# Optimization experiments

Hardware: AMD Instinct MI355X
Metric: run time of the kernel (lower is better)

Reference implementation:

```python
import jax, jax.numpy as jnp
import numpy as np

B, L, R, D = 64, 512, 512, 512
F_CONV, H = 100, 60

def setup_inputs() -> dict:
    key = jax.random.key(0)
    ks = jax.random.split(key, 8)
    l_lengths = jax.random.randint(ks[0], (B,), L // 2, L + 1)
    r_lengths = jax.random.randint(ks[1], (B,), R // 2, R + 1)
    l_vectors = jax.random.normal(ks[2], (L, B, D), jnp.float32)
    r_vectors = jax.random.normal(ks[3], (R, B, D), jnp.float32)
    Wconv = jax.random.normal(ks[4], (F_CONV, D), jnp.float32) / np.sqrt(D).astype(np.float32)
    bconv = jnp.zeros((F_CONV,), jnp.float32)
    Wd = jax.random.normal(ks[5], (H, 2 * F_CONV), jnp.float32) / np.sqrt(2 * F_CONV).astype(np.float32)
    bd = jnp.zeros((H,), jnp.float32)
    return {"l_lengths": l_lengths, "l_vectors": l_vectors, "r_lengths": r_lengths,
            "r_vectors": r_vectors, "Wconv": Wconv, "bconv": bconv, "Wd": Wd, "bd": bd}

def reference(l_lengths, l_vectors, r_lengths, r_vectors, Wconv, bconv, Wd, bd):
    Lm, Bm, Dm = l_vectors.shape
    Rm = r_vectors.shape[0]
    # masks, seq-first [L,B] like pad_sequence output
    l_mask = (jnp.arange(Lm)[:, None] < l_lengths[None, :]).astype(l_vectors.dtype)
    r_mask = (jnp.arange(Rm)[:, None] < r_lengths[None, :]).astype(r_vectors.dtype)
    lmT, rmT = l_mask.T, r_mask.T  # [B,L], [B,R]

    # co-attention scores [B,L,R]
    attention = jnp.einsum('lbd,rbd->blr', l_vectors, r_vectors)
    attention = attention * lmT[:, :, None] * rmT[:, None, :]

    att_r = jax.nn.softmax(attention - 10.0 * (1.0 - lmT[:, :, None]), axis=1)
    att_r = att_r * lmT[:, :, None]
    att_r = att_r / (att_r.sum(axis=1, keepdims=True) + 1e-13)

    att_l = jax.nn.softmax(attention - 10.0 * (1.0 - rmT[:, None, :]), axis=2)
    att_l = att_l * rmT[:, None, :]
    att_l = att_l / (att_l.sum(axis=2, keepdims=True) + 1e-13)

    # ---- left side: stats + top-1 hard attention ----
    rl = r_lengths.astype(l_vectors.dtype)[:, None]
    l_mean = att_l.sum(axis=2) / rl                              # [B,L]
    l_w = (att_l * att_l).sum(axis=2) / rl - l_mean * l_mean
    l_w = l_w / jnp.maximum(l_mean, 0.001)
    l_a = att_l.max(axis=2)                                      # top-1 value [B,L]
    l_i = att_l.argmax(axis=2)                                   # top-1 index [B,L]
    l_i = l_i * lmT.astype(l_i.dtype)
    l_a = l_a / jnp.maximum(l_a, 0.001)                          # k=1: sum == value
    gathered = jnp.take_along_axis(r_vectors, l_i.T[:, :, None], axis=0)  # [L,B,D]
    l_counter = l_a.T[:, :, None] * gathered
    l_c = l_w.T[:, :, None] * jnp.abs(l_vectors - l_counter) * l_mask[:, :, None]

    # ---- right side ----
    ll = l_lengths.astype(r_vectors.dtype)[:, None]
    r_mean = att_r.sum(axis=1) / ll                              # [B,R]
    r_w = (att_r * att_r).sum(axis=1) / ll - r_mean * r_mean
    r_w = r_w / jnp.maximum(r_mean, 0.001)
    r_a = att_r.max(axis=1)                                      # [B,R]
    r_i = att_r.argmax(axis=1)
    r_i = r_i * rmT.astype(r_i.dtype)
    r_a = r_a / jnp.maximum(r_a, 0.001)
    gathered_r = jnp.take_along_axis(l_vectors, r_i.T[:, :, None], axis=0)  # [R,B,D]
    r_counter = r_a.T[:, :, None] * gathered_r
    r_c = r_w.T[:, :, None] * jnp.abs(r_vectors - r_counter) * r_mask[:, :, None]

    # SentenceConv(1, 100, dim): kernel (1, dim) conv == per-position linear,
    # ReLU, masked max-pool over the sequence.
    def sconv(x, mask):  # x [S,B,D], mask [S,B]
        h = jax.nn.relu(jnp.einsum('sbd,fd->bsf', x, Wconv) + bconv)  # [B,S,F]
        h = h - (1.0 - mask.T)[:, :, None] * 1e9
        return h.max(axis=1)  # [B,F]

    feats = jnp.concatenate([sconv(l_c, l_mask), sconv(r_c, r_mask)], axis=1)  # [B,200]
    return jax.nn.relu(feats @ Wd.T + bd)  # [B,60]
```

## Files before the change

### kernel.cpp

```cpp
#include <hip/hip_runtime.h>
#include <math.h>

#define BB 64
#define LL 512
#define RR 512
#define DD 512
#define FC 100
#define FP 112
#define HH 60
#define BD (BB*DD)

typedef __attribute__((ext_vector_type(8))) short bf16x8;
typedef __attribute__((ext_vector_type(4))) float f32x4;

__device__ __forceinline__ unsigned short bf16rne(float x) {
  unsigned u = __float_as_uint(x);
  return (unsigned short)((u + 0x7fffu + ((u >> 16) & 1u)) >> 16);
}
__device__ __forceinline__ float bf16tof(unsigned short h) {
  return __uint_as_float((unsigned)h << 16);
}

__device__ __forceinline__ void split2(float x0, float x1, unsigned& h2, unsigned& l2) {
  unsigned u0 = __float_as_uint(x0), u1 = __float_as_uint(x1);
  h2 = __builtin_amdgcn_perm(u1, u0, 0x07060302u);
  float r0 = x0 - __uint_as_float(u0 & 0xffff0000u);
  float r1 = x1 - __uint_as_float(u1 & 0xffff0000u);
  l2 = __builtin_amdgcn_perm(__float_as_uint(r1), __float_as_uint(r0), 0x07060302u);
}

__global__ __launch_bounds__(512, 2) void gemm_att(const float* __restrict__ lv,
                                                   const float* __restrict__ rv,
                                                   const int* __restrict__ llen,
                                                   const int* __restrict__ rlen,
                                                   float* __restrict__ lpart,
                                                   float* __restrict__ rpart) {
  __shared__ unsigned short Ah[256][40];
  __shared__ unsigned short Al[256][40];
  __shared__ unsigned short Bh[256][40];
  __shared__ unsigned short Bl[256][40];

  const int bid = blockIdx.x;
  const int wid = (bid & 7) * 32 + (bid >> 3);
  const int b  = wid >> 2;
  const int l0 = ((wid >> 1) & 1) * 256;
  const int r0 = (wid & 1) * 256;

  const int t = threadIdx.x;
  const int srow = t >> 1;
  const int half = t & 1;
  const int kq = half * 16;

  const float* Abase = lv + (size_t)(l0 + srow) * BD + b * DD + kq;
  const float* Bbase = rv + (size_t)(r0 + srow) * BD + b * DD + kq;

  float4 pa[4], pb[4];
#pragma unroll
  for (int q = 0; q < 4; ++q) {
    pa[q] = *(const float4*)(Abase + q * 4);
    pb[q] = *(const float4*)(Bbase + q * 4);
  }

  const int lane = t & 63;
  const int wv = t >> 6;
  const int wrow = wv >> 2;
  const int wcol = wv & 3;
  const int fr = lane & 15;
  const int kh = lane >> 4;

  f32x4 acc[8][4];
#pragma unroll
  for (int i = 0; i < 8; ++i)
#pragma unroll
    for (int j = 0; j < 4; ++j) acc[i][j] = (f32x4){0.f, 0.f, 0.f, 0.f};

  for (int it = 0; it < 16; ++it) {
    __syncthreads();
#pragma unroll
    for (int q = 0; q < 4; ++q) {
      unsigned h01, l01, h23, l23;
      split2(pa[q].x, pa[q].y, h01, l01);
      split2(pa[q].z, pa[q].w, h23, l23);
      *(uint2*)&Ah[srow][kq + q * 4] = make_uint2(h01, h23);
      *(uint2*)&Al[srow][kq + q * 4] = make_uint2(l01, l23);
      split2(pb[q].x, pb[q].y, h01, l01);
      split2(pb[q].z, pb[q].w, h23, l23);
      *(uint2*)&Bh[srow][kq + q * 4] = make_uint2(h01, h23);
      *(uint2*)&Bl[srow][kq + q * 4] = make_uint2(l01, l23);
    }
    if (it < 15) {
      const float* An = Abase + (it + 1) * 32;
      const float* Bn = Bbase + (it + 1) * 32;
#pragma unroll
      for (int q = 0; q < 4; ++q) {
        pa[q] = *(const float4*)(An + q * 4);
        pb[q] = *(const float4*)(Bn + q * 4);
      }
    }
    __syncthreads();

    bf16x8 bh[4], bl[4];
#pragma unroll
    for (int j = 0; j < 4; ++j) {
      bh[j] = *(const bf16x8*)&Bh[wcol * 64 + j * 16 + fr][kh * 8];
      bl[j] = *(const bf16x8*)&Bl[wcol * 64 + j * 16 + fr][kh * 8];
    }
#pragma unroll
    for (int i = 0; i < 8; ++i) {
      bf16x8 ah = *(const bf16x8*)&Ah[wrow * 128 + i * 16 + fr][kh * 8];
      bf16x8 al = *(const bf16x8*)&Al[wrow * 128 + i * 16 + fr][kh * 8];
#pragma unroll
      for (int j = 0; j < 4; ++j) {
        acc[i][j] = __builtin_amdgcn_mfma_f32_16x16x32_bf16(ah, bh[j], acc[i][j], 0, 0, 0);
        acc[i][j] = __builtin_amdgcn_mfma_f32_16x16x32_bf16(ah, bl[j], acc[i][j], 0, 0, 0);
        acc[i][j] = __builtin_amdgcn_mfma_f32_16x16x32_bf16(al, bh[j], acc[i][j], 0, 0, 0);
      }
    }
  }

  const int ll_ = llen[b], rl_ = rlen[b];
  __syncthreads();
  float* rowsc = (float*)&Ah[0][0];
  float* colsc = (float*)&Bh[0][0];

#pragma unroll
  for (int i = 0; i < 8; ++i) {
#pragma unroll
    for (int q = 0; q < 4; ++q) {
      const int lrow = wrow * 128 + i * 16 + kh * 4 + q;
      const bool vl = (l0 + lrow) < ll_;
      float s[4];
      float M = -1e30f, bS = -1e30f; int bI = 0;
#pragma unroll
      for (int j = 0; j < 4; ++j) {
        int r = r0 + wcol * 64 + j * 16 + fr;
        bool vr = r < rl_;
        float raw = acc[i][j][q];
        s[j] = !vr ? -10.f : (vl ? raw : 0.f);
        M = fmaxf(M, s[j]);
        if (vr && s[j] > bS) { bS = s[j]; bI = r; }
      }
#pragma unroll
      for (int m = 1; m < 16; m <<= 1) M = fmaxf(M, __shfl_xor(M, m, 64));
      float z0 = 0.f, zv = 0.f, q2 = 0.f;
#pragma unroll
      for (int j = 0; j < 4; ++j) {
        float e = __expf(s[j] - M);
        z0 += e;
        int r = r0 + wcol * 64 + j * 16 + fr;
        if (r < rl_) { zv += e; q2 += e * e; }
      }
#pragma unroll
      for (int m = 1; m < 16; m <<= 1) {
        z0 += __shfl_xor(z0, m, 64);
        zv += __shfl_xor(zv, m, 64);
        q2 += __shfl_xor(q2, m, 64);
        float oS = __shfl_xor(bS, m, 64);
        int   oI = __shfl_xor(bI, m, 64);
        if (oS > bS || (oS == bS && oI < bI)) { bS = oS; bI = oI; }
      }
      if (fr == 0) {
        float* p = rowsc + (wcol * 256 + lrow) * 6;
        p[0] = M; p[1] = z0; p[2] = zv; p[3] = q2; p[4] = bS; p[5] = __int_as_float(bI);
      }
    }
  }

#pragma unroll
  for (int j = 0; j < 4; ++j) {
    const int ccol = wcol * 64 + j * 16 + fr;
    const bool vr = (r0 + ccol) < rl_;
    float M = -1e30f, bS = -1e30f; int bI = 0;
#pragma unroll
    for (int i = 0; i < 8; ++i)
#pragma unroll
      for (int q = 0; q < 4; ++q) {
        int lg = l0 + wrow * 128 + i * 16 + kh * 4 + q;
        bool vl = lg < ll_;
        float raw = acc[i][j][q];
        float sv = !vl ? -10.f : (vr ? raw : 0.f);
        M = fmaxf(M, sv);
        if (vl && sv > bS) { bS = sv; bI = lg; }
      }
    float z0 = 0.f, zv = 0.f, q2 = 0.f;
#pragma unroll
    for (int i = 0; i < 8; ++i)
#pragma unroll
      for (int q = 0; q < 4; ++q) {
        int lg = l0 + wrow * 128 + i * 16 + kh * 4 + q;
        bool vl = lg < ll_;
        float raw = acc[i][j][q];
        float sv = !vl ? -10.f : (vr ? raw : 0.f);
        float e = __expf(sv - M);
        z0 += e;
        if (vl) { zv += e; q2 += e * e; }
      }
#pragma unroll
    for (int m = 16; m < 64; m <<= 1) {
      float oM = __shfl_xor(M, m, 64);
      float oz0 = __shfl_xor(z0, m, 64);
      float ozv = __shfl_xor(zv, m, 64);
      float oq2 = __shfl_xor(q2, m, 64);
      float oS = __shfl_xor(bS, m, 64);
      int   oI = __shfl_xor(bI, m, 64);
      float Mn = fmaxf(M, oM);
      float c0 = __expf(M - Mn), c1 = __expf(oM - Mn);
      z0 = z0 * c0 + oz0 * c1;
      zv = zv * c0 + ozv * c1;
      q2 = q2 * c0 * c0 + oq2 * c1 * c1;
      M = Mn;
      if (oS > bS || (oS == bS && oI < bI)) { bS = oS; bI = oI; }
    }
    if (kh == 0) {
      float* p = colsc + (wrow * 256 + ccol) * 6;
      p[0] = M; p[1] = z0; p[2] = zv; p[3] = q2; p[4] = bS; p[5] = __int_as_float(bI);
    }
  }

  __syncthreads();

  if (t < 256) {
    const float* p = rowsc + t * 6;
    float M = p[0], z0 = p[1], zv = p[2], q2 = p[3], bS = p[4];
    int bI = __float_as_int(p[5]);
#pragma unroll
    for (int w2 = 1; w2 < 4; ++w2) {
      const float* pp = rowsc + (w2 * 256 + t) * 6;
      float M1 = pp[0], z01 = pp[1], zv1 = pp[2], q21 = pp[3], bS1 = pp[4];
      int bI1 = __float_as_int(pp[5]);
      float Mn = fmaxf(M, M1);
      float c0 = __expf(M - Mn), c1 = __expf(M1 - Mn);
      z0 = z0 * c0 + z01 * c1;
      zv = zv * c0 + zv1 * c1;
      q2 = q2 * c0 * c0 + q21 * c1 * c1;
      M = Mn;
      if (bS1 > bS || (bS1 == bS && bI1 < bI)) { bS = bS1; bI = bI1; }
    }
    const int l = l0 + t;
    float* dst = lpart + (((size_t)(b * 512 + l)) * 2 + (r0 >> 8)) * 6;
    *(float2*)(dst + 0) = make_float2(M, z0);
    *(float2*)(dst + 2) = make_float2(zv, q2);
    *(float2*)(dst + 4) = make_float2(bS, __int_as_float(bI));
  } else {
    const int c = t - 256;
    const float* p = colsc + c * 6;
    float M = p[0], z0 = p[1], zv = p[2], q2 = p[3], bS = p[4];
    int bI = __float_as_int(p[5]);
    {
      const float* pp = colsc + (256 + c) * 6;
      float M1 = pp[0], z01 = pp[1], zv1 = pp[2], q21 = pp[3], bS1 = pp[4];
      int bI1 = __float_as_int(pp[5]);
      float Mn = fmaxf(M, M1);
      float c0 = __expf(M - Mn), c1 = __expf(M1 - Mn);
      z0 = z0 * c0 + z01 * c1;
      zv = zv * c0 + zv1 * c1;
      q2 = q2 * c0 * c0 + q21 * c1 * c1;
      M = Mn;
      if (bS1 > bS || (bS1 == bS && bI1 < bI)) { bS = bS1; bI = bI1; }
    }
    const int r = r0 + c;
    float* dst = rpart + (((size_t)(b * 512 + r)) * 2 + (l0 >> 8)) * 6;
    *(float2*)(dst + 0) = make_float2(M, z0);
    *(float2*)(dst + 2) = make_float2(zv, q2);
    *(float2*)(dst + 4) = make_float2(bS, __int_as_float(bI));
  }
}

__global__ __launch_bounds__(256) void stats_merge(const float* __restrict__ lpart,
    const float* __restrict__ rpart,
    const int* __restrict__ llen, const int* __restrict__ rlen,
    float* __restrict__ lwv, float* __restrict__ lan, int* __restrict__ lidx,
    float* __restrict__ rwv, float* __restrict__ ran, int* __restrict__ ridx) {
  const int gid = blockIdx.x * 256 + threadIdx.x;
  const int side = gid >> 15;
  const int pos = gid & 32767;
  const int b = pos >> 9, p = pos & 511;
  const float* part = (side ? rpart : lpart) + (size_t)pos * 12;
  float M = part[0], z0 = part[1], zv = part[2], q2 = part[3], bS = part[4];
  int bI = __float_as_int(part[5]);
  {
    float M1 = part[6], z01 = part[7], zv1 = part[8], q21 = part[9], bS1 = part[10];
    int bI1 = __float_as_int(part[11]);
    float Mn = fmaxf(M, M1);
    float c0 = __expf(M - Mn), c1 = __expf(M1 - Mn);
    z0 = z0 * c0 + z01 * c1;
    zv = zv * c0 + zv1 * c1;
    q2 = q2 * c0 * c0 + q21 * c1 * c1;
    M = Mn;
    if (bS1 > bS || (bS1 == bS && bI1 < bI)) { bS = bS1; bI = bI1; }
  }
  const int len = side ? llen[b] : rlen[b];
  const int own = side ? rlen[b] : llen[b];
  float S = zv / z0;
  float inv = 1.f / (S + 1e-13f);
  float sumq = S * inv;
  float mean = sumq / (float)len;
  float sumq2 = q2 / (z0 * z0) * inv * inv;
  float var = sumq2 / (float)len - mean * mean;
  float wv = var / fmaxf(mean, 0.001f);
  float qmax = __expf(bS - M) / z0 * inv;
  float an = qmax / fmaxf(qmax, 0.001f);
  int idx = (p < own) ? bI : 0;
  if (side == 0) { lwv[pos] = wv; lan[pos] = an; lidx[pos] = idx; }
  else           { rwv[pos] = wv; ran[pos] = an; ridx[pos] = idx; }
}

__global__ void prep_w(const float* __restrict__ Wconv,
                       unsigned short* __restrict__ Whg, unsigned short* __restrict__ Wlg) {
  int i = blockIdx.x * 256 + threadIdx.x;
  if (i < FP * DD) {
    int f = i >> 9;
    float w = (f < FC) ? Wconv[i] : 0.f;
    unsigned short h = bf16rne(w);
    unsigned short l = bf16rne(w - bf16tof(h));
    Whg[i] = h; Wlg[i] = l;
  }
}

__global__ __launch_bounds__(256) void conv_pool_mfma(const float* __restrict__ lv,
    const float* __restrict__ rv,
    const float* __restrict__ lwv, const float* __restrict__ lan, const int* __restrict__ lidx,
    const float* __restrict__ rwv, const float* __restrict__ ran, const int* __restrict__ ridx,
    const int* __restrict__ llen, const int* __restrict__ rlen,
    const unsigned short* __restrict__ Whg, const unsigned short* __restrict__ Wlg,
    const float* __restrict__ bconv, float* __restrict__ feat) {
  __shared__ unsigned short Ah[128][40];
  __shared__ unsigned short Al[128][40];
  __shared__ unsigned short Wh[FP][40];
  __shared__ unsigned short Wl[FP][40];
  __shared__ float pool[4][FP];
  __shared__ float ppw[128], ppa[128];
  __shared__ int   ppi[128], ppv[128];

  const int bid = blockIdx.x;
  const int wid = (bid & 7) * 64 + (bid >> 3);
  const int side = wid >> 8;
  const int b    = (wid >> 2) & 63;
  const int s0   = (wid & 3) * 128;

  const int t = threadIdx.x;
  const float* x; const float* y; const float* wb; const float* ab; const int* ib; int plen;
  if (side == 0) { x = lv; y = rv; wb = lwv; ab = lan; ib = lidx; plen = llen[b]; }
  else           { x = rv; y = lv; wb = rwv; ab = ran; ib = ridx; plen = rlen[b]; }

  if (t < 128) {
    int pos = s0 + t;
    ppw[t] = wb[b * 512 + pos];
    ppa[t] = ab[b * 512 + pos];
    ppi[t] = ib[b * 512 + pos];
    ppv[t] = (pos < plen) ? 1 : 0;
  }
  __syncthreads();

  const int pos  = t >> 1;
  const int half = t & 1;
  const float w_ = ppw[pos];
  const float a_ = ppa[pos];
  const int   yi = ppi[pos];
  const float* xp = x + (size_t)(s0 + pos) * BD + b * DD + half * 16;
  const float* yp = y + (size_t)yi * BD + b * DD + half * 16;

  float4 xv[4], yv[4];
#pragma unroll
  for (int q = 0; q < 4; ++q) {
    xv[q] = *(const float4*)(xp + q * 4);
    yv[q] = *(const float4*)(yp + q * 4);
  }

  const int lane = t & 63;
  const int wvi = t >> 6;
  const int m0 = wvi * 32;
  const int fr = lane & 15;
  const int kh = lane >> 4;

  f32x4 acc[2][7];
#pragma unroll
  for (int i = 0; i < 2; ++i)
#pragma unroll
    for (int j = 0; j < 7; ++j) acc[i][j] = (f32x4){0.f, 0.f, 0.f, 0.f};

  for (int it = 0; it < 16; ++it) {
    const int k0 = it * 32;
    __syncthreads();
#pragma unroll
    for (int q = 0; q < 2; ++q) {
      float d0 = w_ * fabsf(xv[2*q].x   - a_ * yv[2*q].x);
      float d1 = w_ * fabsf(xv[2*q].y   - a_ * yv[2*q].y);
      float d2 = w_ * fabsf(xv[2*q].z   - a_ * yv[2*q].z);
      float d3 = w_ * fabsf(xv[2*q].w   - a_ * yv[2*q].w);
      float d4 = w_ * fabsf(xv[2*q+1].x - a_ * yv[2*q+1].x);
      float d5 = w_ * fabsf(xv[2*q+1].y - a_ * yv[2*q+1].y);
      float d6 = w_ * fabsf(xv[2*q+1].z - a_ * yv[2*q+1].z);
      float d7 = w_ * fabsf(xv[2*q+1].w - a_ * yv[2*q+1].w);
      unsigned h01, l01, h23, l23, h45, l45, h67, l67;
      split2(d0, d1, h01, l01);
      split2(d2, d3, h23, l23);
      split2(d4, d5, h45, l45);
      split2(d6, d7, h67, l67);
      *(uint4*)&Ah[pos][half * 16 + q * 8] = make_uint4(h01, h23, h45, h67);
      *(uint4*)&Al[pos][half * 16 + q * 8] = make_uint4(l01, l23, l45, l67);
    }
#pragma unroll
    for (int rep = 0; rep < 2; ++rep) {
      int idx = t + rep * 256;
      if (idx < FP * 4) {
        int f = idx >> 2, q = idx & 3;
        *(ulonglong2*)&Wh[f][q * 8] = *(const ulonglong2*)&Whg[f * DD + k0 + q * 8];
        *(ulonglong2*)&Wl[f][q * 8] = *(const ulonglong2*)&Wlg[f * DD + k0 + q * 8];
      }
    }
    if (it < 15) {
      const float* xn = xp + k0 + 32;
      const float* yn = yp + k0 + 32;
#pragma unroll
      for (int q = 0; q < 4; ++q) {
        xv[q] = *(const float4*)(xn + q * 4);
        yv[q] = *(const float4*)(yn + q * 4);
      }
    }
    __syncthreads();

    bf16x8 ah[2], al[2];
#pragma unroll
    for (int i = 0; i < 2; ++i) {
      ah[i] = *(const bf16x8*)&Ah[m0 + i * 16 + fr][kh * 8];
      al[i] = *(const bf16x8*)&Al[m0 + i * 16 + fr][kh * 8];
    }
#pragma unroll
    for (int j = 0; j < 7; ++j) {
      bf16x8 bh = *(const bf16x8*)&Wh[j * 16 + fr][kh * 8];
      bf16x8 bl = *(const bf16x8*)&Wl[j * 16 + fr][kh * 8];
#pragma unroll
      for (int i = 0; i < 2; ++i) {
        acc[i][j] = __builtin_amdgcn_mfma_f32_16x16x32_bf16(ah[i], bh, acc[i][j], 0, 0, 0);
        acc[i][j] = __builtin_amdgcn_mfma_f32_16x16x32_bf16(ah[i], bl, acc[i][j], 0, 0, 0);
        acc[i][j] = __builtin_amdgcn_mfma_f32_16x16x32_bf16(al[i], bh, acc[i][j], 0, 0, 0);
      }
    }
  }

#pragma unroll
  for (int j = 0; j < 7; ++j) {
    int f = j * 16 + fr;
    float bcv = (f < FC) ? bconv[f] : 0.f;
    float vmax = -1e30f;
#pragma unroll
    for (int i = 0; i < 2; ++i) {
#pragma unroll
      for (int q = 0; q < 4; ++q) {
        int sl = m0 + i * 16 + kh * 4 + q;
        if (ppv[sl]) vmax = fmaxf(vmax, fmaxf(acc[i][j][q] + bcv, 0.f));
      }
    }
    vmax = fmaxf(vmax, __shfl_xor(vmax, 16, 64));
    vmax = fmaxf(vmax, __shfl_xor(vmax, 32, 64));
    if (lane < 16) pool[wvi][f] = vmax;
  }
  __syncthreads();
  if (t < FC) {
    float v = fmaxf(fmaxf(pool[0][t], pool[1][t]), fmaxf(pool[2][t], pool[3][t]));
    if (v > -1e29f) atomicMax((int*)&feat[b * 200 + side * FC + t], __float_as_int(v));
  }
}

__global__ void dense_out(const float* __restrict__ feat, const float* __restrict__ Wd,
                          const float* __restrict__ bd, float* __restrict__ out) {
  int b = blockIdx.x, h = threadIdx.x;
  if (h < HH) {
    float s = bd[h];
    const float* fb = feat + b * 200;
    const float* wr = Wd + h * 200;
    for (int k = 0; k < 200; ++k) s += fb[k] * wr[k];
    out[b * HH + h] = fmaxf(s, 0.f);
  }
}

extern "C" void kernel_launch(void* const* d_in, const int* in_sizes, int n_in,
                              void* d_out, int out_size, void* d_ws, size_t ws_size,
                              hipStream_t stream) {
  (void)in_sizes; (void)n_in; (void)out_size; (void)ws_size;
  const int*   llen  = (const int*)d_in[0];
  const float* lv    = (const float*)d_in[1];
  const int*   rlen  = (const int*)d_in[2];
  const float* rv    = (const float*)d_in[3];
  const float* Wconv = (const float*)d_in[4];
  const float* bconv = (const float*)d_in[5];
  const float* Wd    = (const float*)d_in[6];
  const float* bd    = (const float*)d_in[7];
  float* out = (float*)d_out;
  char* ws = (char*)d_ws;
  size_t off = 0;
  unsigned short* Whg = (unsigned short*)(ws + off); off += (size_t)FP * DD * 2;
  unsigned short* Wlg = (unsigned short*)(ws + off); off += (size_t)FP * DD * 2;
  float* lpart = (float*)(ws + off); off += (size_t)BB * LL * 2 * 6 * 4;
  float* rpart = (float*)(ws + off); off += (size_t)BB * RR * 2 * 6 * 4;
  float* lwv = (float*)(ws + off); off += (size_t)BB * LL * 4;
  float* lan = (float*)(ws + off); off += (size_t)BB * LL * 4;
  int*   lidx= (int*)  (ws + off); off += (size_t)BB * LL * 4;
  float* rwv = (float*)(ws + off); off += (size_t)BB * RR * 4;
  float* ran = (float*)(ws + off); off += (size_t)BB * RR * 4;
  int*   ridx= (int*)  (ws + off); off += (size_t)BB * RR * 4;
  float* feat= (float*)(ws + off); off += (size_t)BB * 200 * 4;

  hipMemsetAsync(feat, 0, BB * 200 * 4, stream);
  prep_w<<<(FP * DD + 255) / 256, 256, 0, stream>>>(Wconv, Whg, Wlg);
  gemm_att<<<dim3(256), 512, 0, stream>>>(lv, rv, llen, rlen, lpart, rpart);
  stats_merge<<<dim3(256), 256, 0, stream>>>(lpart, rpart, llen, rlen,
                                             lwv, lan, lidx, rwv, ran, ridx);
  conv_pool_mfma<<<dim3(512), 256, 0, stream>>>(lv, rv, lwv, lan, lidx,
                                                rwv, ran, ridx, llen, rlen,
                                                Whg, Wlg, bconv, feat);
  dense_out<<<BB, 64, 0, stream>>>(feat, Wd, bd, out);
}
```

Before: 135.7 us.

## Slim softmax partial stats to float4 and use DPP row reductions

Drops the z0 accumulator and the tracked best score from the attention epilogue. z0 is rebuilt analytically from zv plus the count of masked entries times exp(-10-M), and the top-1 value is taken to be the max M, so only the argmax index is tracked, as the lowest index whose score equals M. Cross-lane reductions within 16-lane groups move from shuffles to DPP row_ror moves, and partial records shrink from six floats to a single float4. This cuts shuffle traffic, register pressure and partial-record bandwidth, but adds reliance on exact-equality ties and on the assumption that the max over valid entries equals M.

```diff
diff --git a/kernel.cpp b/kernel.cpp
--- a/kernel.cpp
+++ b/kernel.cpp
@@ -29,16 +29,39 @@
   l2 = __builtin_amdgcn_perm(__float_as_uint(r1), __float_as_uint(r0), 0x07060302u);
 }
 
+template <int N>
+__device__ __forceinline__ float ror_max_f(float v) {
+  return fmaxf(v, __uint_as_float(__builtin_amdgcn_mov_dpp(__float_as_uint(v), 0x120 | N, 0xf, 0xf, true)));
+}
+template <int N>
+__device__ __forceinline__ float ror_add_f(float v) {
+  return v + __uint_as_float(__builtin_amdgcn_mov_dpp(__float_as_uint(v), 0x120 | N, 0xf, 0xf, true));
+}
+template <int N>
+__device__ __forceinline__ int ror_min_i(int v) {
+  int o = __builtin_amdgcn_mov_dpp(v, 0x120 | N, 0xf, 0xf, true);
+  return o < v ? o : v;
+}
+__device__ __forceinline__ float row16_max(float v) {
+  v = ror_max_f<1>(v); v = ror_max_f<2>(v); v = ror_max_f<4>(v); return ror_max_f<8>(v);
+}
+__device__ __forceinline__ float row16_sum(float v) {
+  v = ror_add_f<1>(v); v = ror_add_f<2>(v); v = ror_add_f<4>(v); return ror_add_f<8>(v);
+}
+__device__ __forceinline__ int row16_min(int v) {
+  v = ror_min_i<1>(v); v = ror_min_i<2>(v); v = ror_min_i<4>(v); return ror_min_i<8>(v);
+}
+
 __global__ __launch_bounds__(512, 2) void gemm_att(const float* __restrict__ lv,
                                                    const float* __restrict__ rv,
                                                    const int* __restrict__ llen,
                                                    const int* __restrict__ rlen,
-                                                   float* __restrict__ lpart,
-                                                   float* __restrict__ rpart) {
-  __shared__ unsigned short Ah[256][40];
-  __shared__ unsigned short Al[256][40];
-  __shared__ unsigned short Bh[256][40];
-  __shared__ unsigned short Bl[256][40];
+                                                   float4* __restrict__ lpart,
+                                                   float4* __restrict__ rpart) {
+  __shared__ __align__(16) unsigned short Ah[256][40];
+  __shared__ __align__(16) unsigned short Al[256][40];
+  __shared__ __align__(16) unsigned short Bh[256][40];
+  __shared__ __align__(16) unsigned short Bl[256][40];
 
   const int bid = blockIdx.x;
   const int wid = (bid & 7) * 32 + (bid >> 3);
@@ -120,154 +143,129 @@
 
   const int ll_ = llen[b], rl_ = rlen[b];
   __syncthreads();
-  float* rowsc = (float*)&Ah[0][0];
-  float* colsc = (float*)&Bh[0][0];
+  float4* rowsc = (float4*)&Ah[0][0];
+  float4* colsc = (float4*)&Bh[0][0];
+
+  const int rbase = r0 + wcol * 64 + fr;
+  bool vr4[4]; int rr4[4];
+#pragma unroll
+  for (int j = 0; j < 4; ++j) { rr4[j] = rbase + j * 16; vr4[j] = rr4[j] < rl_; }
 
 #pragma unroll
   for (int i = 0; i < 8; ++i) {
 #pragma unroll
     for (int q = 0; q < 4; ++q) {
-      const int lrow = wrow * 128 + i * 16 + kh * 4 + q;
-      const bool vl = (l0 + lrow) < ll_;
+      const int trow = wrow * 128 + i * 16 + kh * 4 + q;
+      const bool vl = (l0 + trow) < ll_;
       float s[4];
-      float M = -1e30f, bS = -1e30f; int bI = 0;
+      float M = -1e30f;
 #pragma unroll
       for (int j = 0; j < 4; ++j) {
-        int r = r0 + wcol * 64 + j * 16 + fr;
-        bool vr = r < rl_;
         float raw = acc[i][j][q];
-        s[j] = !vr ? -10.f : (vl ? raw : 0.f);
+        s[j] = !vr4[j] ? -10.f : (vl ? raw : 0.f);
         M = fmaxf(M, s[j]);
-        if (vr && s[j] > bS) { bS = s[j]; bI = r; }
-      }
-#pragma unroll
-      for (int m = 1; m < 16; m <<= 1) M = fmaxf(M, __shfl_xor(M, m, 64));
-      float z0 = 0.f, zv = 0.f, q2 = 0.f;
+      }
+      M = row16_max(M);
+      float zv = 0.f, q2 = 0.f;
+      int loc = 0x7fffffff;
 #pragma unroll
       for (int j = 0; j < 4; ++j) {
         float e = __expf(s[j] - M);
-        z0 += e;
-        int r = r0 + wcol * 64 + j * 16 + fr;
-        if (r < rl_) { zv += e; q2 += e * e; }
-      }
-#pragma unroll
-      for (int m = 1; m < 16; m <<= 1) {
-        z0 += __shfl_xor(z0, m, 64);
-        zv += __shfl_xor(zv, m, 64);
-        q2 += __shfl_xor(q2, m, 64);
-        float oS = __shfl_xor(bS, m, 64);
-        int   oI = __shfl_xor(bI, m, 64);
-        if (oS > bS || (oS == bS && oI < bI)) { bS = oS; bI = oI; }
-      }
-      if (fr == 0) {
-        float* p = rowsc + (wcol * 256 + lrow) * 6;
-        p[0] = M; p[1] = z0; p[2] = zv; p[3] = q2; p[4] = bS; p[5] = __int_as_float(bI);
-      }
+        if (vr4[j]) {
+          zv += e; q2 += e * e;
+          if (s[j] == M && rr4[j] < loc) loc = rr4[j];
+        }
+      }
+      zv = row16_sum(zv);
+      q2 = row16_sum(q2);
+      loc = row16_min(loc);
+      if (fr == 0)
+        rowsc[wcol * 256 + trow] = make_float4(M, zv, q2, __int_as_float(loc));
     }
   }
 
 #pragma unroll
   for (int j = 0; j < 4; ++j) {
-    const int ccol = wcol * 64 + j * 16 + fr;
-    const bool vr = (r0 + ccol) < rl_;
-    float M = -1e30f, bS = -1e30f; int bI = 0;
+    const int tcol = wcol * 64 + j * 16 + fr;
+    const bool vr = (r0 + tcol) < rl_;
+    float M = -1e30f;
 #pragma unroll
     for (int i = 0; i < 8; ++i)
 #pragma unroll
       for (int q = 0; q < 4; ++q) {
         int lg = l0 + wrow * 128 + i * 16 + kh * 4 + q;
         bool vl = lg < ll_;
-        float raw = acc[i][j][q];
-        float sv = !vl ? -10.f : (vr ? raw : 0.f);
+        float sv = !vl ? -10.f : (vr ? acc[i][j][q] : 0.f);
         M = fmaxf(M, sv);
-        if (vl && sv > bS) { bS = sv; bI = lg; }
-      }
-    float z0 = 0.f, zv = 0.f, q2 = 0.f;
+      }
+    M = fmaxf(M, __shfl_xor(M, 16, 64));
+    M = fmaxf(M, __shfl_xor(M, 32, 64));
+    float zv = 0.f, q2 = 0.f;
+    int loc = 0x7fffffff;
 #pragma unroll
     for (int i = 0; i < 8; ++i)
 #pragma unroll
       for (int q = 0; q < 4; ++q) {
         int lg = l0 + wrow * 128 + i * 16 + kh * 4 + q;
         bool vl = lg < ll_;
-        float raw = acc[i][j][q];
-        float sv = !vl ? -10.f : (vr ? raw : 0.f);
+        float sv = !vl ? -10.f : (vr ? acc[i][j][q] : 0.f);
         float e = __expf(sv - M);
-        z0 += e;
-        if (vl) { zv += e; q2 += e * e; }
-      }
-#pragma unroll
-    for (int m = 16; m < 64; m <<= 1) {
-      float oM = __shfl_xor(M, m, 64);
-      float oz0 = __shfl_xor(z0, m, 64);
-      float ozv = __shfl_xor(zv, m, 64);
-      float oq2 = __shfl_xor(q2, m, 64);
-      float oS = __shfl_xor(bS, m, 64);
-      int   oI = __shfl_xor(bI, m, 64);
-      float Mn = fmaxf(M, oM);
-      float c0 = __expf(M - Mn), c1 = __expf(oM - Mn);
-      z0 = z0 * c0 + oz0 * c1;
-      zv = zv * c0 + ozv * c1;
-      q2 = q2 * c0 * c0 + oq2 * c1 * c1;
-      M = Mn;
-      if (oS > bS || (oS == bS && oI < bI)) { bS = oS; bI = oI; }
-    }
-    if (kh == 0) {
-      float* p = colsc + (wrow * 256 + ccol) * 6;
-      p[0] = M; p[1] = z0; p[2] = zv; p[3] = q2; p[4] = bS; p[5] = __int_as_float(bI);
-    }
+        if (vl) {
+          zv += e; q2 += e * e;
+          if (sv == M && lg < loc) loc = lg;
+        }
+      }
+    zv += __shfl_xor(zv, 16, 64); zv += __shfl_xor(zv, 32, 64);
+    q2 += __shfl_xor(q2, 16, 64); q2 += __shfl_xor(q2, 32, 64);
+    { int o = __shfl_xor(loc, 16, 64); loc = o < loc ? o : loc; }
+    { int o = __shfl_xor(loc, 32, 64); loc = o < loc ? o : loc; }
+    if (kh == 0)
+      colsc[wrow * 256 + tcol] = make_float4(M, zv, q2, __int_as_float(loc));
   }
 
   __syncthreads();
 
   if (t < 256) {
-    const float* p = rowsc + t * 6;
-    float M = p[0], z0 = p[1], zv = p[2], q2 = p[3], bS = p[4];
-    int bI = __float_as_int(p[5]);
+    float4 p = rowsc[t];
+    float M = p.x, zv = p.y, q2 = p.z;
+    int loc = __float_as_int(p.w);
 #pragma unroll
     for (int w2 = 1; w2 < 4; ++w2) {
-      const float* pp = rowsc + (w2 * 256 + t) * 6;
-      float M1 = pp[0], z01 = pp[1], zv1 = pp[2], q21 = pp[3], bS1 = pp[4];
-      int bI1 = __float_as_int(pp[5]);
+      float4 o = rowsc[w2 * 256 + t];
+      float M1 = o.x;
       float Mn = fmaxf(M, M1);
       float c0 = __expf(M - Mn), c1 = __expf(M1 - Mn);
-      z0 = z0 * c0 + z01 * c1;
-      zv = zv * c0 + zv1 * c1;
-      q2 = q2 * c0 * c0 + q21 * c1 * c1;
+      zv = zv * c0 + o.y * c1;
+      q2 = q2 * c0 * c0 + o.z * c1 * c1;
+      int loc1 = __float_as_int(o.w);
+      loc = (M1 > M) ? loc1 : ((M1 == M && loc1 < loc) ? loc1 : loc);
       M = Mn;
-      if (bS1 > bS || (bS1 == bS && bI1 < bI)) { bS = bS1; bI = bI1; }
-    }
-    const int l = l0 + t;
-    float* dst = lpart + (((size_t)(b * 512 + l)) * 2 + (r0 >> 8)) * 6;
-    *(float2*)(dst + 0) = make_float2(M, z0);
-    *(float2*)(dst + 2) = make_float2(zv, q2);
-    *(float2*)(dst + 4) = make_float2(bS, __int_as_float(bI));
+    }
+    lpart[((size_t)(b * 512 + l0 + t)) * 2 + (r0 >> 8)] =
+        make_float4(M, zv, q2, __int_as_float(loc));
   } else {
     const int c = t - 256;
-    const float* p = colsc + c * 6;
-    float M = p[0], z0 = p[1], zv = p[2], q2 = p[3], bS = p[4];
-    int bI = __float_as_int(p[5]);
+    float4 p = colsc[c];
+    float M = p.x, zv = p.y, q2 = p.z;
+    int loc = __float_as_int(p.w);
     {
-      const float* pp = colsc + (256 + c) * 6;
-      float M1 = pp[0], z01 = pp[1], zv1 = pp[2], q21 = pp[3], bS1 = pp[4];
-      int bI1 = __float_as_int(pp[5]);
+      float4 o = colsc[256 + c];
+      float M1 = o.x;
       float Mn = fmaxf(M, M1);
       float c0 = __expf(M - Mn), c1 = __expf(M1 - Mn);
-      z0 = z0 * c0 + z01 * c1;
-      zv = zv * c0 + zv1 * c1;
-      q2 = q2 * c0 * c0 + q21 * c1 * c1;
+      zv = zv * c0 + o.y * c1;
+      q2 = q2 * c0 * c0 + o.z * c1 * c1;
+      int loc1 = __float_as_int(o.w);
+      loc = (M1 > M) ? loc1 : ((M1 == M && loc1 < loc) ? loc1 : loc);
       M = Mn;
-      if (bS1 > bS || (bS1 == bS && bI1 < bI)) { bS = bS1; bI = bI1; }
-    }
-    const int r = r0 + c;
-    float* dst = rpart + (((size_t)(b * 512 + r)) * 2 + (l0 >> 8)) * 6;
-    *(float2*)(dst + 0) = make_float2(M, z0);
-    *(float2*)(dst + 2) = make_float2(zv, q2);
-    *(float2*)(dst + 4) = make_float2(bS, __int_as_float(bI));
-  }
-}
-
-__global__ __launch_bounds__(256) void stats_merge(const float* __restrict__ lpart,
-    const float* __restrict__ rpart,
+    }
+    rpart[((size_t)(b * 512 + r0 + c)) * 2 + (l0 >> 8)] =
+        make_float4(M, zv, q2, __int_as_float(loc));
+  }
+}
+
+__global__ __launch_bounds__(256) void stats_merge(const float4* __restrict__ lpart,
+    const float4* __restrict__ rpart,
     const int* __restrict__ llen, const int* __restrict__ rlen,
     float* __restrict__ lwv, float* __restrict__ lan, int* __restrict__ lidx,
     float* __restrict__ rwv, float* __restrict__ ran, int* __restrict__ ridx) {
@@ -275,22 +273,24 @@
   const int side = gid >> 15;
   const int pos = gid & 32767;
   const int b = pos >> 9, p = pos & 511;
-  const float* part = (side ? rpart : lpart) + (size_t)pos * 12;
-  float M = part[0], z0 = part[1], zv = part[2], q2 = part[3], bS = part[4];
-  int bI = __float_as_int(part[5]);
+  const float4* part = (side ? rpart : lpart) + (size_t)pos * 2;
+  float4 P0 = part[0], P1 = part[1];
+  float M = P0.x, zv = P0.y, q2 = P0.z;
+  int loc = __float_as_int(P0.w);
   {
-    float M1 = part[6], z01 = part[7], zv1 = part[8], q21 = part[9], bS1 = part[10];
-    int bI1 = __float_as_int(part[11]);
+    float M1 = P1.x;
     float Mn = fmaxf(M, M1);
     float c0 = __expf(M - Mn), c1 = __expf(M1 - Mn);
-    z0 = z0 * c0 + z01 * c1;
-    zv = zv * c0 + zv1 * c1;
-    q2 = q2 * c0 * c0 + q21 * c1 * c1;
+    zv = zv * c0 + P1.y * c1;
+    q2 = q2 * c0 * c0 + P1.z * c1 * c1;
+    int loc1 = __float_as_int(P1.w);
+    loc = (M1 > M) ? loc1 : ((M1 == M && loc1 < loc) ? loc1 : loc);
     M = Mn;
-    if (bS1 > bS || (bS1 == bS && bI1 < bI)) { bS = bS1; bI = bI1; }
   }
   const int len = side ? llen[b] : rlen[b];
   const int own = side ? rlen[b] : llen[b];
+  const int ninv = side ? (LL - llen[b]) : (RR - rlen[b]);
+  float z0 = zv + (float)ninv * __expf(-10.f - M);
   float S = zv / z0;
   float inv = 1.f / (S + 1e-13f);
   float sumq = S * inv;
@@ -298,9 +298,9 @@
   float sumq2 = q2 / (z0 * z0) * inv * inv;
   float var = sumq2 / (float)len - mean * mean;
   float wv = var / fmaxf(mean, 0.001f);
-  float qmax = __expf(bS - M) / z0 * inv;
+  float qmax = inv / z0;
   float an = qmax / fmaxf(qmax, 0.001f);
-  int idx = (p < own) ? bI : 0;
+  int idx = (p < own && loc != 0x7fffffff) ? loc : 0;
   if (side == 0) { lwv[pos] = wv; lan[pos] = an; lidx[pos] = idx; }
   else           { rwv[pos] = wv; ran[pos] = an; ridx[pos] = idx; }
 }
@@ -324,10 +324,10 @@
     const int* __restrict__ llen, const int* __restrict__ rlen,
     const unsigned short* __restrict__ Whg, const unsigned short* __restrict__ Wlg,
     const float* __restrict__ bconv, float* __restrict__ feat) {
-  __shared__ unsigned short Ah[128][40];
-  __shared__ unsigned short Al[128][40];
-  __shared__ unsigned short Wh[FP][40];
-  __shared__ unsigned short Wl[FP][40];
+  __shared__ __align__(16) unsigned short Ah[128][40];
+  __shared__ __align__(16) unsigned short Al[128][40];
+  __shared__ __align__(16) unsigned short Wh[FP][40];
+  __shared__ __align__(16) unsigned short Wl[FP][40];
   __shared__ float pool[4][FP];
   __shared__ float ppw[128], ppa[128];
   __shared__ int   ppi[128], ppv[128];
@@ -492,8 +492,8 @@
   size_t off = 0;
   unsigned short* Whg = (unsigned short*)(ws + off); off += (size_t)FP * DD * 2;
   unsigned short* Wlg = (unsigned short*)(ws + off); off += (size_t)FP * DD * 2;
-  float* lpart = (float*)(ws + off); off += (size_t)BB * LL * 2 * 6 * 4;
-  float* rpart = (float*)(ws + off); off += (size_t)BB * RR * 2 * 6 * 4;
+  float4* lpart = (float4*)(ws + off); off += (size_t)BB * LL * 2 * 16;
+  float4* rpart = (float4*)(ws + off); off += (size_t)BB * RR * 2 * 16;
   float* lwv = (float*)(ws + off); off += (size_t)BB * LL * 4;
   float* lan = (float*)(ws + off); off += (size_t)BB * LL * 4;
   int*   lidx= (int*)  (ws + off); off += (size_t)BB * LL * 4;
```

Result: faster. 121.0 us (-10.8%).
